# Optimization experiments

Hardware: AMD Instinct MI355X
Metric: run time of the kernel (lower is better)

Reference implementation:

```python
import jax, jax.numpy as jnp
import numpy as np

N = 50000      # num nodes (== num segments for aggregation)
E = 800000     # num edges
D_IN = 128
D_OUT = 128


def setup_inputs() -> dict:
    key = jax.random.key(0)
    k1, k2, k3, k4, k5, k6 = jax.random.split(key, 6)
    x = jax.random.normal(k1, (N, D_IN), dtype=jnp.float32)
    edge_rows = jax.random.randint(k2, (E,), 0, N, dtype=jnp.int32)
    edge_cols = jax.random.randint(k3, (E,), 0, N, dtype=jnp.int32)
    edge_vals = jax.random.uniform(k4, (E,), dtype=jnp.float32)
    stdv = 1.0 / np.sqrt(D_OUT)
    weight = jax.random.uniform(k5, (D_IN, D_OUT), dtype=jnp.float32, minval=-stdv, maxval=stdv)
    root_weight = jax.random.uniform(k6, (D_IN, D_OUT), dtype=jnp.float32, minval=-stdv, maxval=stdv)
    return {"x": x, "edge_rows": edge_rows, "edge_cols": edge_cols,
            "edge_vals": edge_vals, "weight": weight, "root_weight": root_weight}


def reference(x, edge_rows, edge_cols, edge_vals, weight, root_weight):
    # support = x @ W                                  [N, D_OUT]
    support = jnp.dot(x, weight)
    # out = spmm(adj, support): adj in COO form.
    # message per edge: adj[r, c] * support[c]         [E, D_OUT]
    msgs = support[edge_cols] * edge_vals[:, None]
    agg = jax.ops.segment_sum(msgs, edge_rows, num_segments=N)  # [N, D_OUT]
    # out += x @ W_root  (bias=False configuration)
    return agg + jnp.dot(x, root_weight)
```

## Files before the change

kernel.cpp:

```cpp
#include <hip/hip_runtime.h>

#define D 128
#define NCK 512
#define RPB 64
#define CHUNKCAP 1600
#define BCAP 2048
#define SCANW 1024
#define RAWB 20992

typedef short short8 __attribute__((ext_vector_type(8)));
typedef float v4f __attribute__((ext_vector_type(4)));
typedef float float2v __attribute__((ext_vector_type(2)));

static __device__ __forceinline__ unsigned short f2bf(float f) {
    unsigned u = __builtin_bit_cast(unsigned, f);
    u = (u + 0x7FFFu + ((u >> 16) & 1u)) >> 16;
    return (unsigned short)u;
}

__global__ __launch_bounds__(256) void wt_prep(
    const float* __restrict__ W, const float* __restrict__ Wr,
    unsigned short* __restrict__ Wt)
{
    const int gid = (int)blockIdx.x * 256 + (int)threadIdx.x;
    const int k  = gid >> 8;
    const int nn = gid & 255;
    const float v = (nn < D) ? W[k * D + nn] : Wr[k * D + (nn - D)];
    Wt[nn * D + k] = f2bf(v);
}

__global__ __launch_bounds__(256) void prep_gemm(
    const int* __restrict__ rows, const int* __restrict__ cols,
    const float* __restrict__ vals,
    unsigned* __restrict__ pkT, int2* __restrict__ sortedB,
    const float* __restrict__ x, const unsigned short* __restrict__ Wt,
    unsigned short* __restrict__ support, unsigned short* __restrict__ rootbuf,
    int M, int E, int nbuck, int chunk)
{
    __shared__ __align__(16) char raw[RAWB];
    const int t = threadIdx.x;

    if ((int)blockIdx.x < NCK) {
        int* hist = (int*)raw;
        int* cur  = hist + SCANW;
        int2* stg = (int2*)(raw + 2 * SCANW * 4);
        const int c = blockIdx.x;

        #pragma unroll
        for (int j = 0; j < SCANW / 256; ++j) hist[t + j * 256] = 0;
        __syncthreads();

        const int base = c * chunk;
        const int endv = min(base + chunk, E);
        for (int e = base + t; e < endv; e += 256)
            atomicAdd(&hist[rows[e] >> 6], 1);
        __syncthreads();

        int cl_[4];
        #pragma unroll
        for (int j = 0; j < 4; ++j) cl_[j] = hist[t + j * 256];
        for (int off = 1; off < SCANW; off <<= 1) {
            int a[4];
            #pragma unroll
            for (int j = 0; j < 4; ++j) {
                const int idx = t + j * 256;
                a[j] = (idx >= off) ? hist[idx - off] : 0;
            }
            __syncthreads();
            #pragma unroll
            for (int j = 0; j < 4; ++j) hist[t + j * 256] += a[j];
            __syncthreads();
        }
        #pragma unroll
        for (int j = 0; j < 4; ++j) {
            const int idx = t + j * 256;
            const int ex = hist[idx] - cl_[j];
            cur[idx] = ex;
            if (idx < nbuck)
                pkT[(size_t)c * nbuck + idx] =
                    ((unsigned)cl_[j] << 16) | (unsigned)ex;
        }
        __syncthreads();

        for (int e = base + t; e < endv; e += 256) {
            const int r  = rows[e];
            const int cc = cols[e];
            const float v = vals[e];
            const int pos = atomicAdd(&cur[r >> 6], 1);
            stg[pos] = make_int2(((r & (RPB - 1)) << 16) | cc, __float_as_int(v));
        }
        __syncthreads();

        const int n = endv - base;
        for (int k = t; k < n; k += 256)
            sortedB[(size_t)base + k] = stg[k];
        return;
    }

    unsigned short (*As)[136] = (unsigned short (*)[136])raw;
    const int w = t >> 6;
    const int lane = t & 63;
    const int nl = lane & 15, quad = lane >> 4;
    const int rowBase = ((int)blockIdx.x - NCK) * 64;

    {
        const int r = t & 63;
        const int seg = t >> 6;
        const int row = rowBase + r;
        unsigned short tmp[32];
        if (row < M) {
            const float4* src = (const float4*)(x + (size_t)row * D + seg * 32);
            #pragma unroll
            for (int j = 0; j < 8; ++j) {
                const float4 v = src[j];
                tmp[j * 4 + 0] = f2bf(v.x); tmp[j * 4 + 1] = f2bf(v.y);
                tmp[j * 4 + 2] = f2bf(v.z); tmp[j * 4 + 3] = f2bf(v.w);
            }
        } else {
            #pragma unroll
            for (int j = 0; j < 32; ++j) tmp[j] = 0;
        }
        #pragma unroll
        for (int j = 0; j < 4; ++j)
            *(short8*)&As[r][seg * 32 + j * 8] = *(const short8*)&tmp[j * 8];
    }

    short8 bfrag[4][4];
    {
        const unsigned short* wbase = Wt + (size_t)(w * 64 + nl) * D + quad * 8;
        #pragma unroll
        for (int nt = 0; nt < 4; ++nt)
            #pragma unroll
            for (int c = 0; c < 4; ++c)
                bfrag[c][nt] = *(const short8*)(wbase + (size_t)nt * 16 * D + c * 32);
    }
    __syncthreads();

    v4f acc[4][4] = {};
    #pragma unroll
    for (int c = 0; c < 4; ++c) {
        short8 afr[4];
        #pragma unroll
        for (int mt = 0; mt < 4; ++mt)
            afr[mt] = *(const short8*)&As[mt * 16 + nl][c * 32 + quad * 8];
        #pragma unroll
        for (int mt = 0; mt < 4; ++mt)
            #pragma unroll
            for (int nt = 0; nt < 4; ++nt)
                acc[mt][nt] = __builtin_amdgcn_mfma_f32_16x16x32_bf16(
                    afr[mt], bfrag[c][nt], acc[mt][nt], 0, 0, 0);
    }

    const int cbase = (w & 1) * 64;
    unsigned short* dst = (w < 2) ? support : rootbuf;
    #pragma unroll
    for (int mt = 0; mt < 4; ++mt)
        #pragma unroll
        for (int reg = 0; reg < 4; ++reg) {
            const int row = rowBase + mt * 16 + quad * 4 + reg;
            if (row < M) {
                #pragma unroll
                for (int nt = 0; nt < 4; ++nt)
                    dst[(size_t)row * D + cbase + nt * 16 + nl] = f2bf(acc[mt][nt][reg]);
            }
        }
}

__global__ __launch_bounds__(512) void sort_aggregate(
    const unsigned* __restrict__ pkT, const int2* __restrict__ sortedB,
    const unsigned short* __restrict__ support,
    const unsigned short* __restrict__ rootbuf,
    float* __restrict__ out, int M, int nbuck, int chunk)
{
    __shared__ int2 stage[BCAP];
    __shared__ unsigned rowList[BCAP];
    __shared__ int csum[NCK];
    __shared__ int offc[NCK];
    __shared__ int rh[RPB];
    __shared__ int rs[RPB + 1];
    __shared__ int rcur[RPB];
    const int b = blockIdx.x, t = threadIdx.x;

    const unsigned pk = pkT[(size_t)t * nbuck + b];
    const int mycnt = (int)(pk >> 16);
    csum[t] = mycnt;
    offc[t] = (int)(pk & 0xFFFFu);
    __syncthreads();
    for (int off = 1; off < NCK; off <<= 1) {
        const int a = (t >= off) ? csum[t - off] : 0;
        __syncthreads();
        csum[t] += a;
        __syncthreads();
    }
    {
        int dst = csum[t] - mycnt;
        int lim = min(dst + mycnt, BCAP) - dst;
        if (lim < 0) lim = 0;
        const int2* src = sortedB + (size_t)t * chunk + offc[t];
        for (int k = 0; k < lim; ++k) stage[dst + k] = src[k];
    }
    if (t < RPB) rh[t] = 0;
    __syncthreads();

    const int T = min(csum[NCK - 1], BCAP);
    for (int e = t; e < T; e += 512) atomicAdd(&rh[stage[e].x >> 16], 1);
    __syncthreads();
    const int myr = (t < RPB) ? rh[t] : 0;
    for (int off = 1; off < RPB; off <<= 1) {
        int a = 0;
        if (t < RPB && t >= off) a = rh[t - off];
        __syncthreads();
        if (t < RPB) rh[t] += a;
        __syncthreads();
    }
    if (t < RPB) { rs[t] = rh[t] - myr; rcur[t] = rh[t] - myr; }
    if (t == RPB - 1) rs[RPB] = rh[RPB - 1];
    __syncthreads();
    for (int e = t; e < T; e += 512) {
        const int2 ed = stage[e];
        const int rib = ed.x >> 16;
        const int pos = atomicAdd(&rcur[rib], 1);
        rowList[pos] = ((unsigned)f2bf(__int_as_float(ed.y)) << 16)
                     | (unsigned)(ed.x & 0xFFFF);
    }
    __syncthreads();

    const int w = t >> 6, lane = t & 63;
    for (int r = w; r < RPB; r += 8) {
        const int row = b * RPB + r;
        if (row >= M) continue;
        const int s = rs[r], e2 = rs[r + 1];
        float ax = 0.f, ay = 0.f;
        int i = s;

        for (; i + 16 <= e2; i += 16) {
            unsigned d[16];
            #pragma unroll
            for (int j = 0; j < 16; ++j) d[j] = rowList[i + j];
            unsigned p[16];
            #pragma unroll
            for (int j = 0; j < 16; ++j)
                p[j] = *(const unsigned*)(support + (size_t)(d[j] & 0xFFFF) * D + lane * 2);
            #pragma unroll
            for (int j = 0; j < 16; ++j) {
                const float v = __builtin_bit_cast(float, d[j] & 0xFFFF0000u);
                ax += __builtin_bit_cast(float, p[j] << 16) * v;
                ay += __builtin_bit_cast(float, p[j] & 0xFFFF0000u) * v;
            }
        }
        if (i + 8 <= e2) {
            unsigned d[8];
            #pragma unroll
            for (int j = 0; j < 8; ++j) d[j] = rowList[i + j];
            unsigned p[8];
            #pragma unroll
            for (int j = 0; j < 8; ++j)
                p[j] = *(const unsigned*)(support + (size_t)(d[j] & 0xFFFF) * D + lane * 2);
            #pragma unroll
            for (int j = 0; j < 8; ++j) {
                const float v = __builtin_bit_cast(float, d[j] & 0xFFFF0000u);
                ax += __builtin_bit_cast(float, p[j] << 16) * v;
                ay += __builtin_bit_cast(float, p[j] & 0xFFFF0000u) * v;
            }
            i += 8;
        }
        if (i < e2) {
            const int m = e2 - i;
            unsigned d[8];
            #pragma unroll
            for (int j = 0; j < 8; ++j) {
                const int idx = i + (j < m ? j : m - 1);
                const unsigned q = rowList[idx];
                d[j] = (j < m) ? q : (q & 0xFFFFu);
            }
            unsigned p[8];
            #pragma unroll
            for (int j = 0; j < 8; ++j)
                p[j] = *(const unsigned*)(support + (size_t)(d[j] & 0xFFFF) * D + lane * 2);
            #pragma unroll
            for (int j = 0; j < 8; ++j) {
                const float v = __builtin_bit_cast(float, d[j] & 0xFFFF0000u);
                ax += __builtin_bit_cast(float, p[j] << 16) * v;
                ay += __builtin_bit_cast(float, p[j] & 0xFFFF0000u) * v;
            }
        }

        const unsigned pr = *(const unsigned*)(rootbuf + (size_t)row * D + lane * 2);
        float2v ov;
        ov.x = ax + __builtin_bit_cast(float, pr << 16);
        ov.y = ay + __builtin_bit_cast(float, pr & 0xFFFF0000u);
        __builtin_nontemporal_store(ov, (float2v*)(out + (size_t)row * D + lane * 2));
    }
}

extern "C" void kernel_launch(void* const* d_in, const int* in_sizes, int n_in,
                              void* d_out, int out_size, void* d_ws, size_t ws_size,
                              hipStream_t stream) {
    const float* x     = (const float*)d_in[0];
    const int*   erows = (const int*)d_in[1];
    const int*   ecols = (const int*)d_in[2];
    const float* evals = (const float*)d_in[3];
    const float* W     = (const float*)d_in[4];
    const float* Wr    = (const float*)d_in[5];
    float* out = (float*)d_out;

    const int M = in_sizes[0] / D;
    const int E = in_sizes[1];

    const int nbuck = (M + RPB - 1) / RPB;
    const int chunk = (E + NCK - 1) / NCK;
    const int nGemm = (M + 63) / 64;

    unsigned short* support = (unsigned short*)d_ws;
    unsigned short* rootbuf = support + (size_t)M * D;
    unsigned short* Wt      = rootbuf + (size_t)M * D;
    unsigned* pkT   = (unsigned*)(Wt + 2 * D * D);
    int2*  sortedB  = (int2*)(pkT + (size_t)NCK * nbuck);

    wt_prep<<<128, 256, 0, stream>>>(W, Wr, Wt);
    prep_gemm<<<NCK + nGemm, 256, 0, stream>>>(
        erows, ecols, evals, pkT, sortedB, x, Wt, support, rootbuf,
        M, E, nbuck, chunk);
    sort_aggregate<<<nbuck, 512, 0, stream>>>(pkT, sortedB,
                                              support, rootbuf, out, M, nbuck, chunk);
}
```

Measured before the change: 151.4 us.

## Halve rows per bucket, add transposed bucket table, use wave-shuffle scans

Buckets now hold 32 rows instead of 64, which doubles the number of aggregation blocks and halves each block's staging buffers. A new kernel transposes the per-chunk bucket count/offset table so each aggregation block reads its 512 entries contiguously rather than with a stride. The barrier-heavy shared-memory prefix scans in both kernels become wave shuffle scans combined across waves, and the aggregation block drops to 256 threads. This adds one extra kernel launch, a second copy of the table, and a histogram twice as large in the binning blocks.

```diff
diff --git a/kernel.cpp b/kernel.cpp
--- a/kernel.cpp
+++ b/kernel.cpp
@@ -2,11 +2,11 @@
 
 #define D 128
 #define NCK 512
-#define RPB 64
+#define RPB 32
 #define CHUNKCAP 1600
-#define BCAP 2048
-#define SCANW 1024
-#define RAWB 20992
+#define BCAP 1024
+#define SCANW 2048
+#define RAWB 29184
 
 typedef short short8 __attribute__((ext_vector_type(8)));
 typedef float v4f __attribute__((ext_vector_type(4)));
@@ -38,7 +38,9 @@
     int M, int E, int nbuck, int chunk)
 {
     __shared__ __align__(16) char raw[RAWB];
+    __shared__ int wsumK[4];
     const int t = threadIdx.x;
+    const int lane = t & 63, w = t >> 6;
 
     if ((int)blockIdx.x < NCK) {
         int* hist = (int*)raw;
@@ -53,32 +55,33 @@
         const int base = c * chunk;
         const int endv = min(base + chunk, E);
         for (int e = base + t; e < endv; e += 256)
-            atomicAdd(&hist[rows[e] >> 6], 1);
-        __syncthreads();
-
-        int cl_[4];
-        #pragma unroll
-        for (int j = 0; j < 4; ++j) cl_[j] = hist[t + j * 256];
-        for (int off = 1; off < SCANW; off <<= 1) {
-            int a[4];
-            #pragma unroll
-            for (int j = 0; j < 4; ++j) {
-                const int idx = t + j * 256;
-                a[j] = (idx >= off) ? hist[idx - off] : 0;
-            }
-            __syncthreads();
-            #pragma unroll
-            for (int j = 0; j < 4; ++j) hist[t + j * 256] += a[j];
-            __syncthreads();
-        }
-        #pragma unroll
-        for (int j = 0; j < 4; ++j) {
-            const int idx = t + j * 256;
-            const int ex = hist[idx] - cl_[j];
-            cur[idx] = ex;
+            atomicAdd(&hist[rows[e] >> 5], 1);
+        __syncthreads();
+
+        int lv[8];
+        int ssum = 0;
+        #pragma unroll
+        for (int j = 0; j < 8; ++j) { lv[j] = hist[8 * t + j]; ssum += lv[j]; }
+        int s = ssum;
+        #pragma unroll
+        for (int d = 1; d < 64; d <<= 1) {
+            const int u = __shfl_up(s, d);
+            if (lane >= d) s += u;
+        }
+        if (lane == 63) wsumK[w] = s;
+        __syncthreads();
+        int woff = 0;
+        #pragma unroll
+        for (int j = 0; j < 4; ++j) if (j < w) woff += wsumK[j];
+        int run = woff + s - ssum;
+        #pragma unroll
+        for (int j = 0; j < 8; ++j) {
+            const int idx = 8 * t + j;
+            cur[idx] = run;
             if (idx < nbuck)
                 pkT[(size_t)c * nbuck + idx] =
-                    ((unsigned)cl_[j] << 16) | (unsigned)ex;
+                    ((unsigned)lv[j] << 16) | (unsigned)run;
+            run += lv[j];
         }
         __syncthreads();
 
@@ -86,7 +89,7 @@
             const int r  = rows[e];
             const int cc = cols[e];
             const float v = vals[e];
-            const int pos = atomicAdd(&cur[r >> 6], 1);
+            const int pos = atomicAdd(&cur[r >> 5], 1);
             stg[pos] = make_int2(((r & (RPB - 1)) << 16) | cc, __float_as_int(v));
         }
         __syncthreads();
@@ -98,8 +101,6 @@
     }
 
     unsigned short (*As)[136] = (unsigned short (*)[136])raw;
-    const int w = t >> 6;
-    const int lane = t & 63;
     const int nl = lane & 15, quad = lane >> 4;
     const int rowBase = ((int)blockIdx.x - NCK) * 64;
 
@@ -166,57 +167,89 @@
         }
 }
 
-__global__ __launch_bounds__(512) void sort_aggregate(
-    const unsigned* __restrict__ pkT, const int2* __restrict__ sortedB,
+__global__ __launch_bounds__(256) void transpose_pk(
+    const unsigned* __restrict__ pkT, unsigned* __restrict__ pkTt, int nbuck)
+{
+    __shared__ unsigned tile[64][65];
+    const int cb = (int)blockIdx.x & 7;
+    const int bb = (int)blockIdx.x >> 3;
+    const int t = threadIdx.x;
+    for (int i = t; i < 64 * 64; i += 256) {
+        const int lc = i & 63, lr = i >> 6;
+        const int b = bb * 64 + lc, c = cb * 64 + lr;
+        tile[lr][lc] = (b < nbuck) ? pkT[(size_t)c * nbuck + b] : 0u;
+    }
+    __syncthreads();
+    for (int i = t; i < 64 * 64; i += 256) {
+        const int lc = i & 63, lr = i >> 6;
+        const int b = bb * 64 + lr, c = cb * 64 + lc;
+        if (b < nbuck) pkTt[(size_t)b * NCK + c] = tile[lc][lr];
+    }
+}
+
+__global__ __launch_bounds__(256) void sort_aggregate(
+    const unsigned* __restrict__ pkTt, const int2* __restrict__ sortedB,
     const unsigned short* __restrict__ support,
     const unsigned short* __restrict__ rootbuf,
     float* __restrict__ out, int M, int nbuck, int chunk)
 {
     __shared__ int2 stage[BCAP];
     __shared__ unsigned rowList[BCAP];
-    __shared__ int csum[NCK];
-    __shared__ int offc[NCK];
+    __shared__ int wsum[4];
     __shared__ int rh[RPB];
     __shared__ int rs[RPB + 1];
     __shared__ int rcur[RPB];
     const int b = blockIdx.x, t = threadIdx.x;
-
-    const unsigned pk = pkT[(size_t)t * nbuck + b];
-    const int mycnt = (int)(pk >> 16);
-    csum[t] = mycnt;
-    offc[t] = (int)(pk & 0xFFFFu);
-    __syncthreads();
-    for (int off = 1; off < NCK; off <<= 1) {
-        const int a = (t >= off) ? csum[t - off] : 0;
-        __syncthreads();
-        csum[t] += a;
-        __syncthreads();
-    }
+    const int lane = t & 63, w = t >> 6;
+
+    const uint2 pk2 = *(const uint2*)(pkTt + (size_t)b * NCK + 2 * t);
+    const int cnt0 = (int)(pk2.x >> 16), off0 = (int)(pk2.x & 0xFFFFu);
+    const int cnt1 = (int)(pk2.y >> 16), off1 = (int)(pk2.y & 0xFFFFu);
+    int s = cnt0 + cnt1;
+    #pragma unroll
+    for (int d = 1; d < 64; d <<= 1) {
+        const int u = __shfl_up(s, d);
+        if (lane >= d) s += u;
+    }
+    if (lane == 63) wsum[w] = s;
+    __syncthreads();
+    int woff = 0, tot = 0;
+    #pragma unroll
+    for (int j = 0; j < 4; ++j) { const int v = wsum[j]; if (j < w) woff += v; tot += v; }
+    const int incl = woff + s;
+    const int base1 = incl - cnt1;
+    const int base0 = base1 - cnt0;
     {
-        int dst = csum[t] - mycnt;
-        int lim = min(dst + mycnt, BCAP) - dst;
-        if (lim < 0) lim = 0;
-        const int2* src = sortedB + (size_t)t * chunk + offc[t];
-        for (int k = 0; k < lim; ++k) stage[dst + k] = src[k];
+        const int2* src = sortedB + (size_t)(2 * t) * chunk + off0;
+        int lim = min(base0 + cnt0, BCAP) - base0; if (lim < 0) lim = 0;
+        for (int k = 0; k < lim; ++k) stage[base0 + k] = src[k];
+    }
+    {
+        const int2* src = sortedB + (size_t)(2 * t + 1) * chunk + off1;
+        int lim = min(base1 + cnt1, BCAP) - base1; if (lim < 0) lim = 0;
+        for (int k = 0; k < lim; ++k) stage[base1 + k] = src[k];
     }
     if (t < RPB) rh[t] = 0;
     __syncthreads();
 
-    const int T = min(csum[NCK - 1], BCAP);
-    for (int e = t; e < T; e += 512) atomicAdd(&rh[stage[e].x >> 16], 1);
-    __syncthreads();
-    const int myr = (t < RPB) ? rh[t] : 0;
-    for (int off = 1; off < RPB; off <<= 1) {
-        int a = 0;
-        if (t < RPB && t >= off) a = rh[t - off];
-        __syncthreads();
-        if (t < RPB) rh[t] += a;
-        __syncthreads();
-    }
-    if (t < RPB) { rs[t] = rh[t] - myr; rcur[t] = rh[t] - myr; }
-    if (t == RPB - 1) rs[RPB] = rh[RPB - 1];
-    __syncthreads();
-    for (int e = t; e < T; e += 512) {
+    const int T = min(tot, BCAP);
+    for (int e = t; e < T; e += 256) atomicAdd(&rh[stage[e].x >> 16], 1);
+    __syncthreads();
+    if (t < 64) {
+        const int mine = (t < RPB) ? rh[t] : 0;
+        int v = mine;
+        #pragma unroll
+        for (int d = 1; d < RPB; d <<= 1) {
+            const int u = __shfl_up(v, d);
+            if (lane >= d) v += u;
+        }
+        if (t < RPB) {
+            rs[t] = v - mine; rcur[t] = v - mine;
+            if (t == RPB - 1) rs[RPB] = v;
+        }
+    }
+    __syncthreads();
+    for (int e = t; e < T; e += 256) {
         const int2 ed = stage[e];
         const int rib = ed.x >> 16;
         const int pos = atomicAdd(&rcur[rib], 1);
@@ -225,13 +258,12 @@
     }
     __syncthreads();
 
-    const int w = t >> 6, lane = t & 63;
-    for (int r = w; r < RPB; r += 8) {
+    for (int r = w; r < RPB; r += 4) {
         const int row = b * RPB + r;
         if (row >= M) continue;
-        const int s = rs[r], e2 = rs[r + 1];
+        const int st = rs[r], e2 = rs[r + 1];
         float ax = 0.f, ay = 0.f;
-        int i = s;
+        int i = st;
 
         for (; i + 16 <= e2; i += 16) {
             unsigned d[16];
@@ -315,12 +347,16 @@
     unsigned short* rootbuf = support + (size_t)M * D;
     unsigned short* Wt      = rootbuf + (size_t)M * D;
     unsigned* pkT   = (unsigned*)(Wt + 2 * D * D);
-    int2*  sortedB  = (int2*)(pkT + (size_t)NCK * nbuck);
+    unsigned* pkTt  = pkT + (size_t)NCK * nbuck;
+    int2*  sortedB  = (int2*)(pkTt + (size_t)nbuck * NCK);
+
+    const int nTb = (nbuck + 63) / 64;
 
     wt_prep<<<128, 256, 0, stream>>>(W, Wr, Wt);
     prep_gemm<<<NCK + nGemm, 256, 0, stream>>>(
         erows, ecols, evals, pkT, sortedB, x, Wt, support, rootbuf,
         M, E, nbuck, chunk);
-    sort_aggregate<<<nbuck, 512, 0, stream>>>(pkT, sortedB,
+    transpose_pk<<<8 * nTb, 256, 0, stream>>>(pkT, pkTt, nbuck);
+    sort_aggregate<<<nbuck, 256, 0, stream>>>(pkTt, sortedB,
                                               support, rootbuf, out, M, nbuck, chunk);
 }
```

Measured after the change: 153.1 us. No clear change (+1.1%).
